# Kernel optimization log

Measured on AMD Instinct MI355X. Metric: run time of the kernel, lower is better.

Reference implementation:

```python
import jax, jax.numpy as jnp
import numpy as np

B, T, H, O = 256, 2048, 64, 2


def setup_inputs() -> dict:
    key = jax.random.key(0)
    ks = jax.random.split(key, 14)
    def lin(k, out_f, in_f):
        bound = np.sqrt(6.0 / (in_f + out_f))
        return jax.random.uniform(k, (out_f, in_f), jnp.float32, -bound, bound)
    return {
        "x": jax.random.normal(ks[0], (B, T, 2), jnp.float32),
        "h0": jax.random.normal(ks[1], (1, B, H), jnp.float32),
        "Wa": lin(ks[2], H, H + 1), "ba": jnp.zeros((H,), jnp.float32),
        "Wp1": lin(ks[3], H, H + 1), "bp1": jnp.zeros((H,), jnp.float32),
        "Wp2": lin(ks[4], H, H + 1), "bp2": jnp.zeros((H,), jnp.float32),
        "Wf": lin(ks[5], H, 2 * H), "bf": jnp.zeros((H,), jnp.float32),
        "Wg": lin(ks[6], H, 2 * H), "bg": jnp.zeros((H,), jnp.float32),
        "Wo": lin(ks[7], O, H), "bo": jnp.zeros((O,), jnp.float32),
    }


def reference(x, h0, Wa, ba, Wp1, bp1, Wp2, bp2, Wf, bf, Wg, bg, Wo, bo):
    # x: [B, T, 2] (I/Q), h0: [1, B, H]
    xt = jnp.swapaxes(x, 0, 1)  # [T, B, 2]

    def step(h, x_t):
        i = x_t[:, 0:1]
        q = x_t[:, 1:2]
        amp = jnp.sqrt(i * i + q * q)
        theta = jnp.arctan2(q, i)
        cos_t = jnp.cos(theta)
        sin_t = jnp.sin(theta)
        a = jnp.tanh(jnp.concatenate([h, amp], -1) @ Wa.T + ba)
        p1 = jnp.tanh(jnp.concatenate([h, cos_t], -1) @ Wp1.T + bp1)
        p2 = jnp.tanh(jnp.concatenate([h, sin_t], -1) @ Wp2.T + bp2)
        u = a * p1 * p2 * (1 - a) * (1 - p1) * (1 - p2)
        hu = jnp.concatenate([h, u], -1)
        f = jax.nn.sigmoid(hu @ Wf.T + bf)
        g = jnp.tanh(hu @ Wg.T + bg)
        h_new = f * h + (1 - f) * g
        y = h_new @ Wo.T + bo
        return h_new, y

    _, ys = jax.lax.scan(step, h0[0], xt)  # ys: [T, B, O]
    return jnp.swapaxes(ys, 0, 1)  # [B, T, O]
```

## Files before the change

kernel.cpp:

```cpp
#include <hip/hip_runtime.h>
#include <math.h>

#define BB 256
#define TT 2048
#define HH 64

typedef _Float16 half2v __attribute__((ext_vector_type(2)));
typedef __fp16  fp16v2 __attribute__((ext_vector_type(2)));
typedef _Float16 half8  __attribute__((ext_vector_type(8)));
typedef float    f32x4  __attribute__((ext_vector_type(4)));
union H2I { half2v h; unsigned int i; };
union F8  { half8 h; uint4 u; };

#if __has_builtin(__builtin_amdgcn_rcpf)
__device__ __forceinline__ float fast_rcp(float v) { return __builtin_amdgcn_rcpf(v); }
#else
__device__ __forceinline__ float fast_rcp(float v) { return 1.0f / v; }
#endif
#if __has_builtin(__builtin_amdgcn_rsqf)
__device__ __forceinline__ float fast_rsq(float v) { return __builtin_amdgcn_rsqf(v); }
#else
__device__ __forceinline__ float fast_rsq(float v) { return rsqrtf(v); }
#endif

__device__ __forceinline__ float tanh_fast(float v) {
    float e = __expf(2.0f * v);
    return fmaf(-2.0f, fast_rcp(e + 1.0f), 1.0f);
}
__device__ __forceinline__ float sigmoid_fast(float v) {
    return fast_rcp(1.0f + __expf(-v));
}
__device__ __forceinline__ float fdot2(half2v a, half2v b, float c) {
    return __builtin_amdgcn_fdot2(a, b, c, false);
}
__device__ __forceinline__ half2v pack_pair(float a, float b) {
    fp16v2 r = __builtin_amdgcn_cvt_pkrtz(a, b);
    return __builtin_bit_cast(half2v, r);
}
__device__ __forceinline__ unsigned pack_u32(float a, float b) {
    fp16v2 r = __builtin_amdgcn_cvt_pkrtz(a, b);
    return __builtin_bit_cast(unsigned, r);
}
__device__ __forceinline__ void pin_h2(half2v& v) {
    H2I u; u.h = v;
    asm volatile("" : "+v"(u.i));
    v = u.h;
}
__device__ __forceinline__ void pin_f8(half8& v) {
    F8 f; f.h = v;
    asm volatile("" : "+v"(f.u.x), "+v"(f.u.y), "+v"(f.u.z), "+v"(f.u.w));
    v = f.h;
}
__device__ __forceinline__ half2v bcast_pair(half2v v, int lane) {
    H2I u; u.h = v;
    H2I w; w.i = __builtin_amdgcn_readlane(u.i, lane);
    return w.h;
}
__device__ __forceinline__ float dpp_neighbor(float v) {
    return __int_as_float(__builtin_amdgcn_mov_dpp(__float_as_int(v), 0xB1, 0xf, 0xf, true));
}
__device__ __forceinline__ half8 make_frag(const float* p) {
    F8 f;
    f.u.x = pack_u32(p[0], p[1]);
    f.u.y = pack_u32(p[2], p[3]);
    f.u.z = pack_u32(p[4], p[5]);
    f.u.w = pack_u32(p[6], p[7]);
    return f.h;
}

__global__ __launch_bounds__(64, 1)
void pgjanet_kernel(const float* __restrict__ x,
                    const float* __restrict__ h0,
                    const float* __restrict__ Wa,  const float* __restrict__ ba,
                    const float* __restrict__ Wp1, const float* __restrict__ bp1,
                    const float* __restrict__ Wp2, const float* __restrict__ bp2,
                    const float* __restrict__ Wf,  const float* __restrict__ bf,
                    const float* __restrict__ Wg,  const float* __restrict__ bg,
                    const float* __restrict__ Wo,  const float* __restrict__ bo,
                    float* __restrict__ out)
{
    const int b = blockIdx.x;
    const int j = threadIdx.x;
    const int c   = j & 15;
    const int grp = j >> 4;

    __shared__ float4 xt[TT];
    __shared__ float  hbuf[64][HH + 1];
    __shared__ float  woLDS[2 * HH];
    __shared__ __align__(16) unsigned int hpk[32];
    __shared__ __align__(16) unsigned int upk[32];

    for (int t = j; t < TT; t += 64) {
        float2 xi = reinterpret_cast<const float2*>(x)[(size_t)b * TT + t];
        float r2 = xi.x * xi.x + xi.y * xi.y;
        float rq = fast_rsq(r2);
        bool ok = r2 > 0.f;
        xt[t] = make_float4(ok ? r2 * rq : 0.f, ok ? xi.x * rq : 1.f,
                            ok ? xi.y * rq : 0.f, 0.f);
    }
    for (int i = j; i < 2 * HH; i += 64) woLDS[i] = Wo[i];

    half8 WB[3][4][2];
    half8 UBf[4][2];
    {
        const float* WsrcA[3] = {Wa, Wp1, Wp2};
#pragma unroll
        for (int g = 0; g < 3; ++g)
#pragma unroll
            for (int tau = 0; tau < 4; ++tau)
#pragma unroll
                for (int kt = 0; kt < 2; ++kt)
                    WB[g][tau][kt] = make_frag(WsrcA[g] + (size_t)(16 * tau + c) * (HH + 1) + 32 * kt + grp * 8);
#pragma unroll
        for (int tau = 0; tau < 4; ++tau)
#pragma unroll
            for (int kt = 0; kt < 2; ++kt)
                UBf[tau][kt] = make_frag(Wf + (size_t)(16 * tau + c) * (2 * HH) + HH + 32 * kt + grp * 8);
#pragma unroll
        for (int g = 0; g < 3; ++g)
#pragma unroll
            for (int tau = 0; tau < 4; ++tau)
#pragma unroll
                for (int kt = 0; kt < 2; ++kt) pin_f8(WB[g][tau][kt]);
#pragma unroll
        for (int tau = 0; tau < 4; ++tau)
#pragma unroll
            for (int kt = 0; kt < 2; ++kt) pin_f8(UBf[tau][kt]);
    }

    half2v wfh[32], wgh[32], wgu[32];
    {
        const float* rf = Wf + (size_t)j * (2 * HH);
        const float* rg = Wg + (size_t)j * (2 * HH);
#pragma unroll
        for (int m = 0; m < 32; ++m) {
            wfh[m] = pack_pair(rf[2 * m], rf[2 * m + 1]);
            wgh[m] = pack_pair(rg[2 * m], rg[2 * m + 1]);
            wgu[m] = pack_pair(rg[HH + 2 * m], rg[HH + 2 * m + 1]);
        }
#pragma unroll
        for (int m = 0; m < 32; ++m) { pin_h2(wfh[m]); pin_h2(wgh[m]); pin_h2(wgu[m]); }
    }

    const float waX  = Wa [j * (HH + 1) + HH];
    const float wp1X = Wp1[j * (HH + 1) + HH];
    const float wp2X = Wp2[j * (HH + 1) + HH];
    const float ba_r = ba[j], bp1_r = bp1[j], bp2_r = bp2[j];
    const float bf_r = bf[j], bg_r = bg[j];
    const float bo0  = bo[0], bo1 = bo[1];

    float  h  = h0[b * HH + j];
    float* yp = out + (size_t)b * (TT * 2);

    __syncthreads();

    const bool b4 = (j & 16) != 0, b5 = (j & 32) != 0;
    const f32x4 zz = {0.f, 0.f, 0.f, 0.f};
    float4 xv = xt[0];

    for (int t = 0; t < TT; ++t) {
        const int tn = (t + 1 < TT) ? (t + 1) : t;
        float4 xv_n = xt[tn];

        float hn = dpp_neighbor(h);
        half2v hp = pack_pair(h, hn);
        {
            H2I w_; w_.h = hp;
            if ((j & 1) == 0) hpk[j >> 1] = w_.i;
        }
        F8 a0u, a1u;
        a0u.u = *reinterpret_cast<const uint4*>(&hpk[grp * 4]);
        a1u.u = *reinterpret_cast<const uint4*>(&hpk[16 + grp * 4]);

        float F0 = bf_r, F1 = 0.f, G0 = bg_r, G1 = 0.f;
#pragma unroll
        for (int m = 0; m < 16; ++m) {
            half2v s0 = bcast_pair(hp, 2 * m);
            half2v s1 = bcast_pair(hp, 2 * (m + 16));
            F0 = fdot2(s0, wfh[m],      F0);
            F1 = fdot2(s1, wfh[m + 16], F1);
            G0 = fdot2(s0, wgh[m],      G0);
            G1 = fdot2(s1, wgh[m + 16], G1);
        }
        float accF = F0 + F1;
        float accG = G0 + G1;

        half8 hA0 = a0u.h, hA1 = a1u.h;
        f32x4 accA[3][4];
#pragma unroll
        for (int g = 0; g < 3; ++g)
#pragma unroll
            for (int tau = 0; tau < 4; ++tau) {
                accA[g][tau] = __builtin_amdgcn_mfma_f32_16x16x32_f16(hA0, WB[g][tau][0], zz, 0, 0, 0);
                accA[g][tau] = __builtin_amdgcn_mfma_f32_16x16x32_f16(hA1, WB[g][tau][1], accA[g][tau], 0, 0, 0);
            }

        float pre[3];
#pragma unroll
        for (int g = 0; g < 3; ++g) {
            float s01 = b4 ? accA[g][1][0] : accA[g][0][0];
            float s23 = b4 ? accA[g][3][0] : accA[g][2][0];
            pre[g] = b5 ? s23 : s01;
        }
        float av = tanh_fast(pre[0] + fmaf(xv.x, waX,  ba_r));
        float p1 = tanh_fast(pre[1] + fmaf(xv.y, wp1X, bp1_r));
        float p2 = tanh_fast(pre[2] + fmaf(xv.z, wp2X, bp2_r));
        float u = fmaf(-av, av, av) * fmaf(-p1, p1, p1) * fmaf(-p2, p2, p2);

        float un = dpp_neighbor(u);
        half2v up = pack_pair(u, un);
        {
            H2I w_; w_.h = up;
            if ((j & 1) == 0) upk[j >> 1] = w_.i;
        }
        F8 u0u, u1u;
        u0u.u = *reinterpret_cast<const uint4*>(&upk[grp * 4]);
        u1u.u = *reinterpret_cast<const uint4*>(&upk[16 + grp * 4]);

        float Gu0 = accG, Gu1 = 0.f;
#pragma unroll
        for (int m = 0; m < 16; ++m) {
            half2v s0 = bcast_pair(up, 2 * m);
            half2v s1 = bcast_pair(up, 2 * (m + 16));
            Gu0 = fdot2(s0, wgu[m],      Gu0);
            Gu1 = fdot2(s1, wgu[m + 16], Gu1);
        }

        half8 uA0 = u0u.h, uA1 = u1u.h;
        f32x4 accCf[4];
#pragma unroll
        for (int tau = 0; tau < 4; ++tau) {
            accCf[tau] = __builtin_amdgcn_mfma_f32_16x16x32_f16(uA0, UBf[tau][0], zz, 0, 0, 0);
            accCf[tau] = __builtin_amdgcn_mfma_f32_16x16x32_f16(uA1, UBf[tau][1], accCf[tau], 0, 0, 0);
        }
        float fs01 = b4 ? accCf[1][0] : accCf[0][0];
        float fs23 = b4 ? accCf[3][0] : accCf[2][0];
        float fu   = b5 ? fs23 : fs01;

        float f = sigmoid_fast(accF + fu);
        float g = tanh_fast(Gu0 + Gu1);
        h = fmaf(f, h - g, g);

        hbuf[t & 63][j] = h;

        if ((t & 63) == 63) {
            float y0 = bo0, y1 = bo1;
#pragma unroll 4
            for (int k = 0; k < HH; ++k) {
                float hv = hbuf[j][k];
                y0 = fmaf(hv, woLDS[k],      y0);
                y1 = fmaf(hv, woLDS[HH + k], y1);
            }
            reinterpret_cast<float2*>(yp)[(t - 63) + j] = make_float2(y0, y1);
        }

        xv = xv_n;
    }
}

extern "C" void kernel_launch(void* const* d_in, const int* in_sizes, int n_in,
                              void* d_out, int out_size, void* d_ws, size_t ws_size,
                              hipStream_t stream) {
    const float* x   = (const float*)d_in[0];
    const float* h0  = (const float*)d_in[1];
    const float* Wa  = (const float*)d_in[2];
    const float* ba  = (const float*)d_in[3];
    const float* Wp1 = (const float*)d_in[4];
    const float* bp1 = (const float*)d_in[5];
    const float* Wp2 = (const float*)d_in[6];
    const float* bp2 = (const float*)d_in[7];
    const float* Wf  = (const float*)d_in[8];
    const float* bf  = (const float*)d_in[9];
    const float* Wg  = (const float*)d_in[10];
    const float* bg  = (const float*)d_in[11];
    const float* Wo  = (const float*)d_in[12];
    const float* bo  = (const float*)d_in[13];
    float* out = (float*)d_out;

    pgjanet_kernel<<<dim3(BB), dim3(64), 0, stream>>>(
        x, h0, Wa, ba, Wp1, bp1, Wp2, bp2, Wf, bf, Wg, bg, Wo, bo, out);
}
```

Measured before the change: 1.711 ms.

## Move Wf/Wg hidden and Wg input matvecs from fdot2 readlane loops onto MFMA

Replaces the per-lane fdot2 dot products, which use readlane broadcasts for the h-part of Wf and Wg and the u-part of Wg, with MFMA 16x16x32 fragments. All five gates now share one MFMA batch on h, and the u-part for f and g is accumulated on top of it. The MFMA issue is also reordered so each gate's first half-K pass runs before any second half-K pass, which lengthens the gap between dependent accumulations. This removes many scalar readlane and fdot2 instructions from the serial recurrence, at the cost of extra MFMA work (most of each 16x16 result is discarded) and more fragment registers.

```diff
diff --git a/kernel.cpp b/kernel.cpp
--- a/kernel.cpp
+++ b/kernel.cpp
@@ -30,9 +30,6 @@
 __device__ __forceinline__ float sigmoid_fast(float v) {
     return fast_rcp(1.0f + __expf(-v));
 }
-__device__ __forceinline__ float fdot2(half2v a, half2v b, float c) {
-    return __builtin_amdgcn_fdot2(a, b, c, false);
-}
 __device__ __forceinline__ half2v pack_pair(float a, float b) {
     fp16v2 r = __builtin_amdgcn_cvt_pkrtz(a, b);
     return __builtin_bit_cast(half2v, r);
@@ -40,21 +37,11 @@
 __device__ __forceinline__ unsigned pack_u32(float a, float b) {
     fp16v2 r = __builtin_amdgcn_cvt_pkrtz(a, b);
     return __builtin_bit_cast(unsigned, r);
-}
-__device__ __forceinline__ void pin_h2(half2v& v) {
-    H2I u; u.h = v;
-    asm volatile("" : "+v"(u.i));
-    v = u.h;
 }
 __device__ __forceinline__ void pin_f8(half8& v) {
     F8 f; f.h = v;
     asm volatile("" : "+v"(f.u.x), "+v"(f.u.y), "+v"(f.u.z), "+v"(f.u.w));
     v = f.h;
-}
-__device__ __forceinline__ half2v bcast_pair(half2v v, int lane) {
-    H2I u; u.h = v;
-    H2I w; w.i = __builtin_amdgcn_readlane(u.i, lane);
-    return w.h;
 }
 __device__ __forceinline__ float dpp_neighbor(float v) {
     return __int_as_float(__builtin_amdgcn_mov_dpp(__float_as_int(v), 0xB1, 0xf, 0xf, true));
@@ -100,46 +87,37 @@
     }
     for (int i = j; i < 2 * HH; i += 64) woLDS[i] = Wo[i];
 
-    half8 WB[3][4][2];
-    half8 UBf[4][2];
+    half8 WB5[5][4][2];
+    half8 UB[2][4][2];
     {
-        const float* WsrcA[3] = {Wa, Wp1, Wp2};
-#pragma unroll
-        for (int g = 0; g < 3; ++g)
+        const float* Wsrc5[5] = {Wa, Wp1, Wp2, Wf, Wg};
+        const int    ld5[5]   = {HH + 1, HH + 1, HH + 1, 2 * HH, 2 * HH};
+#pragma unroll
+        for (int g = 0; g < 5; ++g)
 #pragma unroll
             for (int tau = 0; tau < 4; ++tau)
 #pragma unroll
                 for (int kt = 0; kt < 2; ++kt)
-                    WB[g][tau][kt] = make_frag(WsrcA[g] + (size_t)(16 * tau + c) * (HH + 1) + 32 * kt + grp * 8);
-#pragma unroll
-        for (int tau = 0; tau < 4; ++tau)
-#pragma unroll
-            for (int kt = 0; kt < 2; ++kt)
-                UBf[tau][kt] = make_frag(Wf + (size_t)(16 * tau + c) * (2 * HH) + HH + 32 * kt + grp * 8);
-#pragma unroll
-        for (int g = 0; g < 3; ++g)
-#pragma unroll
-            for (int tau = 0; tau < 4; ++tau)
-#pragma unroll
-                for (int kt = 0; kt < 2; ++kt) pin_f8(WB[g][tau][kt]);
-#pragma unroll
-        for (int tau = 0; tau < 4; ++tau)
-#pragma unroll
-            for (int kt = 0; kt < 2; ++kt) pin_f8(UBf[tau][kt]);
-    }
-
-    half2v wfh[32], wgh[32], wgu[32];
-    {
-        const float* rf = Wf + (size_t)j * (2 * HH);
-        const float* rg = Wg + (size_t)j * (2 * HH);
-#pragma unroll
-        for (int m = 0; m < 32; ++m) {
-            wfh[m] = pack_pair(rf[2 * m], rf[2 * m + 1]);
-            wgh[m] = pack_pair(rg[2 * m], rg[2 * m + 1]);
-            wgu[m] = pack_pair(rg[HH + 2 * m], rg[HH + 2 * m + 1]);
-        }
-#pragma unroll
-        for (int m = 0; m < 32; ++m) { pin_h2(wfh[m]); pin_h2(wgh[m]); pin_h2(wgu[m]); }
+                    WB5[g][tau][kt] = make_frag(Wsrc5[g] + (size_t)(16 * tau + c) * ld5[g] + 32 * kt + grp * 8);
+#pragma unroll
+        for (int g2 = 0; g2 < 2; ++g2)
+#pragma unroll
+            for (int tau = 0; tau < 4; ++tau)
+#pragma unroll
+                for (int kt = 0; kt < 2; ++kt)
+                    UB[g2][tau][kt] = make_frag((g2 ? Wg : Wf) + (size_t)(16 * tau + c) * (2 * HH) + HH + 32 * kt + grp * 8);
+#pragma unroll
+        for (int g = 0; g < 5; ++g)
+#pragma unroll
+            for (int tau = 0; tau < 4; ++tau)
+#pragma unroll
+                for (int kt = 0; kt < 2; ++kt) pin_f8(WB5[g][tau][kt]);
+#pragma unroll
+        for (int g2 = 0; g2 < 2; ++g2)
+#pragma unroll
+            for (int tau = 0; tau < 4; ++tau)
+#pragma unroll
+                for (int kt = 0; kt < 2; ++kt) pin_f8(UB[g2][tau][kt]);
     }
 
     const float waX  = Wa [j * (HH + 1) + HH];
@@ -171,29 +149,23 @@
         F8 a0u, a1u;
         a0u.u = *reinterpret_cast<const uint4*>(&hpk[grp * 4]);
         a1u.u = *reinterpret_cast<const uint4*>(&hpk[16 + grp * 4]);
-
-        float F0 = bf_r, F1 = 0.f, G0 = bg_r, G1 = 0.f;
-#pragma unroll
-        for (int m = 0; m < 16; ++m) {
-            half2v s0 = bcast_pair(hp, 2 * m);
-            half2v s1 = bcast_pair(hp, 2 * (m + 16));
-            F0 = fdot2(s0, wfh[m],      F0);
-            F1 = fdot2(s1, wfh[m + 16], F1);
-            G0 = fdot2(s0, wgh[m],      G0);
-            G1 = fdot2(s1, wgh[m + 16], G1);
-        }
-        float accF = F0 + F1;
-        float accG = G0 + G1;
-
         half8 hA0 = a0u.h, hA1 = a1u.h;
-        f32x4 accA[3][4];
-#pragma unroll
-        for (int g = 0; g < 3; ++g)
-#pragma unroll
-            for (int tau = 0; tau < 4; ++tau) {
-                accA[g][tau] = __builtin_amdgcn_mfma_f32_16x16x32_f16(hA0, WB[g][tau][0], zz, 0, 0, 0);
-                accA[g][tau] = __builtin_amdgcn_mfma_f32_16x16x32_f16(hA1, WB[g][tau][1], accA[g][tau], 0, 0, 0);
-            }
+
+        float xa = fmaf(xv.x, waX,  ba_r);
+        float xp1 = fmaf(xv.y, wp1X, bp1_r);
+        float xp2 = fmaf(xv.z, wp2X, bp2_r);
+
+        f32x4 accA[5][4];
+#pragma unroll
+        for (int g = 0; g < 5; ++g)
+#pragma unroll
+            for (int tau = 0; tau < 4; ++tau)
+                accA[g][tau] = __builtin_amdgcn_mfma_f32_16x16x32_f16(hA0, WB5[g][tau][0], zz, 0, 0, 0);
+#pragma unroll
+        for (int g = 0; g < 5; ++g)
+#pragma unroll
+            for (int tau = 0; tau < 4; ++tau)
+                accA[g][tau] = __builtin_amdgcn_mfma_f32_16x16x32_f16(hA1, WB5[g][tau][1], accA[g][tau], 0, 0, 0);
 
         float pre[3];
 #pragma unroll
@@ -202,9 +174,9 @@
             float s23 = b4 ? accA[g][3][0] : accA[g][2][0];
             pre[g] = b5 ? s23 : s01;
         }
-        float av = tanh_fast(pre[0] + fmaf(xv.x, waX,  ba_r));
-        float p1 = tanh_fast(pre[1] + fmaf(xv.y, wp1X, bp1_r));
-        float p2 = tanh_fast(pre[2] + fmaf(xv.z, wp2X, bp2_r));
+        float av = tanh_fast(pre[0] + xa);
+        float p1 = tanh_fast(pre[1] + xp1);
+        float p2 = tanh_fast(pre[2] + xp2);
         float u = fmaf(-av, av, av) * fmaf(-p1, p1, p1) * fmaf(-p2, p2, p2);
 
         float un = dpp_neighbor(u);
@@ -216,29 +188,25 @@
         F8 u0u, u1u;
         u0u.u = *reinterpret_cast<const uint4*>(&upk[grp * 4]);
         u1u.u = *reinterpret_cast<const uint4*>(&upk[16 + grp * 4]);
-
-        float Gu0 = accG, Gu1 = 0.f;
-#pragma unroll
-        for (int m = 0; m < 16; ++m) {
-            half2v s0 = bcast_pair(up, 2 * m);
-            half2v s1 = bcast_pair(up, 2 * (m + 16));
-            Gu0 = fdot2(s0, wgu[m],      Gu0);
-            Gu1 = fdot2(s1, wgu[m + 16], Gu1);
-        }
-
         half8 uA0 = u0u.h, uA1 = u1u.h;
-        f32x4 accCf[4];
-#pragma unroll
-        for (int tau = 0; tau < 4; ++tau) {
-            accCf[tau] = __builtin_amdgcn_mfma_f32_16x16x32_f16(uA0, UBf[tau][0], zz, 0, 0, 0);
-            accCf[tau] = __builtin_amdgcn_mfma_f32_16x16x32_f16(uA1, UBf[tau][1], accCf[tau], 0, 0, 0);
-        }
-        float fs01 = b4 ? accCf[1][0] : accCf[0][0];
-        float fs23 = b4 ? accCf[3][0] : accCf[2][0];
-        float fu   = b5 ? fs23 : fs01;
-
-        float f = sigmoid_fast(accF + fu);
-        float g = tanh_fast(Gu0 + Gu1);
+
+#pragma unroll
+        for (int g2 = 0; g2 < 2; ++g2)
+#pragma unroll
+            for (int tau = 0; tau < 4; ++tau)
+                accA[3 + g2][tau] = __builtin_amdgcn_mfma_f32_16x16x32_f16(uA0, UB[g2][tau][0], accA[3 + g2][tau], 0, 0, 0);
+#pragma unroll
+        for (int g2 = 0; g2 < 2; ++g2)
+#pragma unroll
+            for (int tau = 0; tau < 4; ++tau)
+                accA[3 + g2][tau] = __builtin_amdgcn_mfma_f32_16x16x32_f16(uA1, UB[g2][tau][1], accA[3 + g2][tau], 0, 0, 0);
+
+        float fs01 = b4 ? accA[3][1][0] : accA[3][0][0];
+        float fs23 = b4 ? accA[3][3][0] : accA[3][2][0];
+        float gs01 = b4 ? accA[4][1][0] : accA[4][0][0];
+        float gs23 = b4 ? accA[4][3][0] : accA[4][2][0];
+        float f = sigmoid_fast((b5 ? fs23 : fs01) + bf_r);
+        float g = tanh_fast((b5 ? gs23 : gs01) + bg_r);
         h = fmaf(f, h - g, g);
 
         hbuf[t & 63][j] = h;
```

Result: faster. 1.505 ms (-12.0%).
